# Kernel optimization log

Hardware: AMD Instinct MI355X
Metric: run time of the kernel (lower is better)

Reference implementation:

```python
import jax, jax.numpy as jnp
import numpy as np

B, T, C = 4, 2048, 1024
H = 16
D = C // H  # head_dim = 64


def setup_inputs() -> dict:
    key = jax.random.key(0)
    ks = jax.random.split(key, 11)
    s = 0.02
    return {
        "q": jax.random.normal(ks[0], (B, T, C), jnp.float32),
        "k": jax.random.normal(ks[1], (B, T, C), jnp.float32),
        "v": jax.random.normal(ks[2], (B, T, C), jnp.float32),
        "Wq": jax.random.normal(ks[3], (C, C), jnp.float32) * s,
        "bq": jnp.zeros((C,), jnp.float32),
        "Wk": jax.random.normal(ks[4], (C, C), jnp.float32) * s,
        "bk": jnp.zeros((C,), jnp.float32),
        "Wv": jax.random.normal(ks[5], (C, C), jnp.float32) * s,
        "bv": jnp.zeros((C,), jnp.float32),
        "Wo": jax.random.normal(ks[6], (C, C), jnp.float32) * s,
        "bo": jnp.zeros((C,), jnp.float32),
    }


def reference(q, k, v, Wq, bq, Wk, bk, Wv, bv, Wo, bo):
    # projections (torch Linear: x @ W.T + b)
    qh = (q @ Wq.T + bq).reshape(B, T, H, D).transpose(0, 2, 1, 3)  # [B,H,T,D]
    kh = (k @ Wk.T + bk).reshape(B, T, H, D).transpose(0, 2, 1, 3)
    vh = (v @ Wv.T + bv).reshape(B, T, H, D).transpose(0, 2, 1, 3)
    scores = jnp.einsum('bhqd,bhkd->bhqk', qh, kh) * (D ** -0.5)  # [B,H,T,T]
    # causal mask (is_causal=True)
    causal = jnp.tril(jnp.ones((T, T), bool))
    scores = jnp.where(causal, scores, -jnp.inf)
    probs = jax.nn.softmax(scores, axis=-1)
    # dropout_rate=0.0 -> identity in eval mode
    out = jnp.einsum('bhqk,bhkd->bhqd', probs, vh)  # [B,H,T,D]
    out = out.transpose(0, 2, 1, 3).reshape(B, T, C)
    return out @ Wo.T + bo
```

## Files before the change

### kernel.cpp

```cpp
#include <hip/hip_runtime.h>
#include <hip/hip_bf16.h>

typedef __attribute__((ext_vector_type(8))) short bf16x8;
typedef __attribute__((ext_vector_type(4))) float f32x4;
typedef __attribute__((ext_vector_type(16))) float f32x16;

__device__ __forceinline__ unsigned short f2bf(float x) {
  union { float f; unsigned u; } v; v.f = x;
  unsigned r = v.u + 0x7fffu + ((v.u >> 16) & 1u);
  return (unsigned short)(r >> 16);
}

__device__ __forceinline__ unsigned cvtpk_bf16(float lo, float hi) {
  unsigned r;
  asm("v_cvt_pk_bf16_f32 %0, %1, %2" : "=v"(r) : "v"(lo), "v"(hi));
  return r;
}
__device__ __forceinline__ void pl32swap(unsigned &a, unsigned &b) {
  asm volatile("v_permlane32_swap_b32 %0, %1" : "+v"(a), "+v"(b));
}
__device__ __forceinline__ void gload_lds16(const void* g, void* l) {
  __builtin_amdgcn_global_load_lds((const __attribute__((address_space(1))) void*)g,
                                   (__attribute__((address_space(3))) void*)l, 16, 0, 0);
}

#define SWZ(x) ((x) ^ ((((x) >> 7) & 7) << 4))

__global__ __launch_bounds__(256) void cvt_w(
    const float* __restrict__ W0, const float* __restrict__ W1,
    const float* __restrict__ W2, const float* __restrict__ W3,
    unsigned short* __restrict__ o0, unsigned short* __restrict__ o1,
    unsigned short* __restrict__ o2, unsigned short* __restrict__ o3,
    float s0) {
  const int z = blockIdx.y;
  const float* W = (z == 0) ? W0 : (z == 1) ? W1 : (z == 2) ? W2 : W3;
  unsigned short* o = (z == 0) ? o0 : (z == 1) ? o1 : (z == 2) ? o2 : o3;
  const float s = (z == 0) ? s0 : 1.0f;
  const int i = blockIdx.x * 256 + threadIdx.x;
  const float4 x = ((const float4*)W)[i];
  uint2 u;
  u.x = cvtpk_bf16(x.x * s, x.y * s);
  u.y = cvtpk_bf16(x.z * s, x.w * s);
  ((uint2*)o)[i] = u;
}

__global__ __launch_bounds__(256) void cvt_x(
    const float* __restrict__ q, const float* __restrict__ k,
    const float* __restrict__ v,
    unsigned short* __restrict__ oq, unsigned short* __restrict__ ok,
    unsigned short* __restrict__ ov) {
  const int z = blockIdx.y;
  const float* X = (z == 0) ? q : (z == 1) ? k : v;
  unsigned short* o = (z == 0) ? oq : (z == 1) ? ok : ov;
  const int i = blockIdx.x * 256 + threadIdx.x;
  const float4 x = ((const float4*)X)[i];
  uint2 u;
  u.x = cvtpk_bf16(x.x, x.y);
  u.y = cvtpk_bf16(x.z, x.w);
  ((uint2*)o)[i] = u;
}

__global__ __launch_bounds__(256) void proj_gemm3(
    const unsigned short* __restrict__ X0, const unsigned short* __restrict__ X1,
    const unsigned short* __restrict__ X2,
    const unsigned short* __restrict__ W0b, const unsigned short* __restrict__ W1b,
    const unsigned short* __restrict__ W2b,
    const float* __restrict__ b0, const float* __restrict__ b1, const float* __restrict__ b2,
    unsigned short* __restrict__ o0, unsigned short* __restrict__ o1,
    unsigned short* __restrict__ o2) {
  const int K = 1024;
  const int NK = 16;
  __shared__ __align__(16) unsigned short As[2][8192];
  __shared__ __align__(16) unsigned short Bs[2][8192];
  const int z = blockIdx.z;
  const unsigned short* A = (z == 0) ? X0 : (z == 1) ? X1 : X2;
  const unsigned short* Wb = (z == 0) ? W0b : (z == 1) ? W1b : W2b;
  const float* bias = (z == 0) ? b0 : (z == 1) ? b1 : b2;
  unsigned short* out = (z == 0) ? o0 : (z == 1) ? o1 : o2;
  const float bscale = (z == 0) ? 0.125f * 1.4426950408889634f : 1.0f;
  const int vtrans = (z == 2);

  const int tid = threadIdx.x;
  const int row0 = blockIdx.x * 128;
  const int col0 = blockIdx.y * 128;
  const int lane = tid & 63;
  const int w = tid >> 6;
  const int wm = (w >> 1) * 64, wn = (w & 1) * 64;
  const int fr = lane & 15;
  const int g = lane >> 4;
  const int frh = fr >> 1;
  const int gcf = ((fr & 1) * 4 + g) ^ frh;
  const int aoff = wm * 64 + frh * 128 + gcf * 16;
  const int boff = wn * 64 + frh * 128 + gcf * 16;

  const unsigned short* asrc[2];
  const unsigned short* bsrc[2];
  int ldo[2];
#pragma unroll
  for (int j = 0; j < 2; ++j) {
    const int L = (w * 2 + j) * 64 + lane;
    const int pp = L >> 3, gc = L & 7;
    const int e = gc ^ (pp & 7);
    const int r = pp * 2 + (e >> 2), c = e & 3;
    asrc[j] = A + (size_t)(row0 + r) * K + c * 8;
    bsrc[j] = Wb + (size_t)(col0 + r) * K + c * 8;
    ldo[j] = (w * 2 + j) * 1024;
  }

  f32x4 acc[4][4] = {};

  auto stage = [&](int buf, int kt) {
#pragma unroll
    for (int h = 0; h < 2; ++h)
#pragma unroll
      for (int j = 0; j < 2; ++j) {
        gload_lds16(asrc[j] + kt * 64 + h * 32, (char*)As[buf] + h * 8192 + ldo[j]);
        gload_lds16(bsrc[j] + kt * 64 + h * 32, (char*)Bs[buf] + h * 8192 + ldo[j]);
      }
  };

  stage(0, 0);
  __syncthreads();
  for (int kt = 0; kt < NK; ++kt) {
    const int buf = kt & 1;
    if (kt + 1 < NK) stage(buf ^ 1, kt + 1);
#pragma unroll
    for (int h = 0; h < 2; ++h) {
      const char* Ab = (const char*)As[buf] + h * 8192;
      const char* Bb = (const char*)Bs[buf] + h * 8192;
      bf16x8 af[4], bfv[4];
#pragma unroll
      for (int i = 0; i < 4; ++i) {
        af[i] = *(const bf16x8*)(Ab + aoff + i * 1024);
        bfv[i] = *(const bf16x8*)(Bb + boff + i * 1024);
      }
      __builtin_amdgcn_s_setprio(1);
#pragma unroll
      for (int i = 0; i < 4; ++i)
#pragma unroll
        for (int j = 0; j < 4; ++j)
          acc[i][j] = __builtin_amdgcn_mfma_f32_16x16x32_bf16(af[i], bfv[j], acc[i][j], 0, 0, 0);
      __builtin_amdgcn_s_setprio(0);
    }
    __syncthreads();
  }

#pragma unroll
  for (int j = 0; j < 4; ++j) {
    const int n = col0 + wn + j * 16 + fr;
    const float bv = bias[n] * bscale;
    const int h = n >> 6, d = n & 63;
#pragma unroll
    for (int i = 0; i < 4; ++i) {
      const int mrow = row0 + wm + i * 16 + g * 4;
      const int b = mrow >> 11, t0 = mrow & 2047;
      if (vtrans) {
        uint2 u;
        u.x = cvtpk_bf16(acc[i][j][0] + bv, acc[i][j][1] + bv);
        u.y = cvtpk_bf16(acc[i][j][2] + bv, acc[i][j][3] + bv);
        *(uint2*)(&out[(((size_t)b * 16 + h) * 64 + d) * 2048 + t0]) = u;
      } else {
#pragma unroll
        for (int r = 0; r < 4; ++r)
          out[(((size_t)b * 16 + h) * 2048 + (t0 + r)) * 64 + d] = f2bf(acc[i][j][r] + bv);
      }
    }
  }
}

__global__ __launch_bounds__(256) void out_gemm(
    const unsigned short* __restrict__ A, const unsigned short* __restrict__ Wb,
    const float* __restrict__ bias, float* __restrict__ out) {
  const int K = 1024;
  const int NK = 16;
  __shared__ __align__(16) unsigned short As[2][8192];
  __shared__ __align__(16) unsigned short Bs[2][8192];
  const int tid = threadIdx.x;
  const int row0 = blockIdx.x * 128;
  const int col0 = blockIdx.y * 128;
  const int lane = tid & 63;
  const int w = tid >> 6;
  const int wm = (w >> 1) * 64, wn = (w & 1) * 64;
  const int fr = lane & 15;
  const int g = lane >> 4;
  const int frh = fr >> 1;
  const int gcf = ((fr & 1) * 4 + g) ^ frh;
  const int aoff = wm * 64 + frh * 128 + gcf * 16;
  const int boff = wn * 64 + frh * 128 + gcf * 16;

  const unsigned short* asrc[2];
  const unsigned short* bsrc[2];
  int ldo[2];
#pragma unroll
  for (int j = 0; j < 2; ++j) {
    const int L = (w * 2 + j) * 64 + lane;
    const int pp = L >> 3, gc = L & 7;
    const int e = gc ^ (pp & 7);
    const int r = pp * 2 + (e >> 2), c = e & 3;
    asrc[j] = A + (size_t)(row0 + r) * K + c * 8;
    bsrc[j] = Wb + (size_t)(col0 + r) * K + c * 8;
    ldo[j] = (w * 2 + j) * 1024;
  }

  f32x4 acc[4][4] = {};

  auto stage = [&](int buf, int kt) {
#pragma unroll
    for (int h = 0; h < 2; ++h)
#pragma unroll
      for (int j = 0; j < 2; ++j) {
        gload_lds16(asrc[j] + kt * 64 + h * 32, (char*)As[buf] + h * 8192 + ldo[j]);
        gload_lds16(bsrc[j] + kt * 64 + h * 32, (char*)Bs[buf] + h * 8192 + ldo[j]);
      }
  };

  stage(0, 0);
  __syncthreads();
  for (int kt = 0; kt < NK; ++kt) {
    const int buf = kt & 1;
    if (kt + 1 < NK) stage(buf ^ 1, kt + 1);
#pragma unroll
    for (int h = 0; h < 2; ++h) {
      const char* Ab = (const char*)As[buf] + h * 8192;
      const char* Bb = (const char*)Bs[buf] + h * 8192;
      bf16x8 af[4], bfv[4];
#pragma unroll
      for (int i = 0; i < 4; ++i) {
        af[i] = *(const bf16x8*)(Ab + aoff + i * 1024);
        bfv[i] = *(const bf16x8*)(Bb + boff + i * 1024);
      }
      __builtin_amdgcn_s_setprio(1);
#pragma unroll
      for (int i = 0; i < 4; ++i)
#pragma unroll
        for (int j = 0; j < 4; ++j)
          acc[i][j] = __builtin_amdgcn_mfma_f32_16x16x32_bf16(af[i], bfv[j], acc[i][j], 0, 0, 0);
      __builtin_amdgcn_s_setprio(0);
    }
    __syncthreads();
  }

#pragma unroll
  for (int j = 0; j < 4; ++j) {
    const int n = col0 + wn + j * 16 + fr;
    const float bv = bias[n];
#pragma unroll
    for (int i = 0; i < 4; ++i) {
      const int mrow = row0 + wm + i * 16 + g * 4;
#pragma unroll
      for (int r = 0; r < 4; ++r)
        out[(size_t)(mrow + r) * 1024 + n] = acc[i][j][r] + bv;
    }
  }
}

__global__ __launch_bounds__(256) void attn_mfma(
    const unsigned short* __restrict__ qh, const unsigned short* __restrict__ kh,
    const unsigned short* __restrict__ vT, unsigned short* __restrict__ Ob) {
  __shared__ __align__(16) unsigned short Klds[2][64 * 64];
  __shared__ __align__(16) unsigned short Vlds[2][64 * 64];

  const int tid = threadIdx.x;
  const int lane = tid & 63;
  const int w = tid >> 6;
  const int bh = blockIdx.y;
  const int b = bh >> 4, h = bh & 15;
  const int q32 = lane & 31;
  const int hi = lane >> 5;

  const char* kbase = (const char*)(kh + (size_t)bh * 2048 * 64);
  const char* vbase = (const char*)(vT + (size_t)bh * 64 * 2048);

  const int lrow = lane >> 3;
  const int cb = (((lane & 7) ^ lrow) << 4);

  auto stage = [&](int buf, int t) {
    const int kv0 = t * 64;
#pragma unroll
    for (int j = 0; j < 2; ++j) {
      const int c = w * 2 + j;
      const int r = c * 8 + lrow;
      gload_lds16(kbase + (size_t)(kv0 + r) * 128 + cb,
                  (char*)Klds[buf] + c * 1024);
      gload_lds16(vbase + (size_t)r * 4096 + (size_t)kv0 * 2 + cb,
                  (char*)Vlds[buf] + c * 1024);
    }
  };

  const int x = (int)blockIdx.x;
  const int qt = (x < 8) ? (15 - x) : (x - 8);
  const int qb = qt * 128 + w * 32;
  const int nt = 2 * qt + 2;

  bf16x8 qf[4];
  {
    const unsigned short* qp = qh + ((size_t)bh * 2048 + qb + q32) * 64;
#pragma unroll
    for (int kk = 0; kk < 4; ++kk)
      qf[kk] = *(const bf16x8*)(qp + kk * 16 + hi * 8);
  }

  f32x16 acc_o[2] = {};
  float l_run = 0.f;

  stage(0, 0);
  __syncthreads();

  int cur = 0;
  for (int t = 0; t < nt; ++t) {
    const int kv0 = t * 64;
    if (t + 1 < nt) stage(cur ^ 1, t + 1);

    if (kv0 < qb + 32) {
      const char* Kb = (const char*)Klds[cur];
      const char* Vb = (const char*)Vlds[cur];

      f32x16 sacc[2] = {};
      __builtin_amdgcn_s_setprio(1);
#pragma unroll
      for (int kk = 0; kk < 4; ++kk) {
        bf16x8 kf0 = *(const bf16x8*)(Kb + SWZ((q32) * 128 + kk * 32 + hi * 16));
        bf16x8 kf1 = *(const bf16x8*)(Kb + SWZ((32 + q32) * 128 + kk * 32 + hi * 16));
        sacc[0] = __builtin_amdgcn_mfma_f32_32x32x16_bf16(kf0, qf[kk], sacc[0], 0, 0, 0);
        sacc[1] = __builtin_amdgcn_mfma_f32_32x32x16_bf16(kf1, qf[kk], sacc[1], 0, 0, 0);
      }
      __builtin_amdgcn_s_setprio(0);

      if (kv0 + 64 > qb) {
        const int qa = qb + q32;
#pragma unroll
        for (int mkv = 0; mkv < 2; ++mkv)
#pragma unroll
          for (int r = 0; r < 16; ++r) {
            const int kva = kv0 + mkv * 32 + 4 * hi + (r & 3) + 8 * (r >> 2);
            if (kva > qa) sacc[mkv][r] = -INFINITY;
          }
      }

      float ls = 0.f;
      unsigned W[2][8];
#pragma unroll
      for (int mkv = 0; mkv < 2; ++mkv)
#pragma unroll
        for (int s = 0; s < 8; ++s) {
          const float p0 = exp2f(sacc[mkv][2 * s]);
          const float p1 = exp2f(sacc[mkv][2 * s + 1]);
          ls += p0 + p1;
          W[mkv][s] = cvtpk_bf16(p0, p1);
        }
      ls += __shfl_xor(ls, 32);
      l_run += ls;

#pragma unroll
      for (int mkv = 0; mkv < 2; ++mkv) {
        pl32swap(W[mkv][0], W[mkv][2]);
        pl32swap(W[mkv][1], W[mkv][3]);
        pl32swap(W[mkv][4], W[mkv][6]);
        pl32swap(W[mkv][5], W[mkv][7]);
      }

      __builtin_amdgcn_s_setprio(1);
#pragma unroll
      for (int wg = 0; wg < 4; ++wg) {
        union { unsigned u[4]; bf16x8 v; } pk;
        pk.u[0] = W[wg >> 1][(wg & 1) * 4 + 0];
        pk.u[1] = W[wg >> 1][(wg & 1) * 4 + 1];
        pk.u[2] = W[wg >> 1][(wg & 1) * 4 + 2];
        pk.u[3] = W[wg >> 1][(wg & 1) * 4 + 3];
        bf16x8 vf0 = *(const bf16x8*)(Vb + SWZ((q32) * 128 + wg * 32 + hi * 16));
        bf16x8 vf1 = *(const bf16x8*)(Vb + SWZ((32 + q32) * 128 + wg * 32 + hi * 16));
        acc_o[0] = __builtin_amdgcn_mfma_f32_32x32x16_bf16(vf0, pk.v, acc_o[0], 0, 0, 0);
        acc_o[1] = __builtin_amdgcn_mfma_f32_32x32x16_bf16(vf1, pk.v, acc_o[1], 0, 0, 0);
      }
      __builtin_amdgcn_s_setprio(0);
    }

    __syncthreads();
    cur ^= 1;
  }

  {
    const float inv = 1.0f / l_run;
    const int qa = qb + q32;
    unsigned short* op = Ob + ((size_t)b * 2048 + qa) * 1024 + h * 64;
#pragma unroll
    for (int md = 0; md < 2; ++md)
#pragma unroll
      for (int rr = 0; rr < 4; ++rr) {
        uint2 u;
        u.x = cvtpk_bf16(acc_o[md][rr * 4 + 0] * inv, acc_o[md][rr * 4 + 1] * inv);
        u.y = cvtpk_bf16(acc_o[md][rr * 4 + 2] * inv, acc_o[md][rr * 4 + 3] * inv);
        *(uint2*)(op + md * 32 + rr * 8 + hi * 4) = u;
      }
  }
}

extern "C" void kernel_launch(void* const* d_in, const int* in_sizes, int n_in,
                              void* d_out, int out_size, void* d_ws, size_t ws_size,
                              hipStream_t stream) {
  (void)in_sizes; (void)n_in; (void)out_size; (void)ws_size;
  const float* q = (const float*)d_in[0];
  const float* k = (const float*)d_in[1];
  const float* v = (const float*)d_in[2];
  const float* Wq = (const float*)d_in[3];
  const float* bq = (const float*)d_in[4];
  const float* Wk = (const float*)d_in[5];
  const float* bk = (const float*)d_in[6];
  const float* Wv = (const float*)d_in[7];
  const float* bv = (const float*)d_in[8];
  const float* Wo = (const float*)d_in[9];
  const float* bo = (const float*)d_in[10];
  float* out = (float*)d_out;

  const size_t SZ = (size_t)4 * 16 * 2048 * 64;
  const size_t WSZ = (size_t)1024 * 1024;
  unsigned short* qx = (unsigned short*)d_ws;
  unsigned short* kx = qx + SZ;
  unsigned short* vx = kx + SZ;
  unsigned short* qh = vx + SZ;
  unsigned short* kh = qh + SZ;
  unsigned short* vT = kh + SZ;
  unsigned short* Wqb = vT + SZ;
  unsigned short* Wkb = Wqb + WSZ;
  unsigned short* Wvb = Wkb + WSZ;
  unsigned short* Wob = Wvb + WSZ;
  unsigned short* Ob = qx;

  dim3 g0(1024, 4), b0(256);
  cvt_w<<<g0, b0, 0, stream>>>(Wq, Wk, Wv, Wo, Wqb, Wkb, Wvb, Wob,
                               0.125f * 1.4426950408889634f);
  dim3 gx(8192, 3), bx(256);
  cvt_x<<<gx, bx, 0, stream>>>(q, k, v, qx, kx, vx);

  dim3 g1(64, 8, 3), b1(256);
  proj_gemm3<<<g1, b1, 0, stream>>>(qx, kx, vx, Wqb, Wkb, Wvb, bq, bk, bv,
                                    qh, kh, vT);

  dim3 g2(16, 64), b2(256);
  attn_mfma<<<g2, b2, 0, stream>>>(qh, kh, vT, Ob);

  dim3 g3(64, 8), b3(256);
  out_gemm<<<g3, b3, 0, stream>>>(Ob, Wob, bo, out);
}
```

Before: 248.3 us.

## Split causal attention KV range across two blocks and combine partials

Each attention block now covers a pair of query tiles (one long, one short) but only half of each tile's KV range, so the two halves run in separate blocks. Unnormalized partial outputs are stored in bf16 along with the row sums, and a new combine kernel adds the halves and normalizes. The intent is better load balance across blocks for the causal workload. In exchange it adds an extra kernel launch, the global traffic for the partials, and a second bf16 rounding of the unnormalized accumulators.

```diff
diff --git a/kernel.cpp b/kernel.cpp
--- a/kernel.cpp
+++ b/kernel.cpp
@@ -10,6 +10,8 @@
   unsigned r = v.u + 0x7fffu + ((v.u >> 16) & 1u);
   return (unsigned short)(r >> 16);
 }
+__device__ __forceinline__ float bflo(unsigned u) { union { unsigned v; float f; } x; x.v = u << 16; return x.f; }
+__device__ __forceinline__ float bfhi(unsigned u) { union { unsigned v; float f; } x; x.v = u & 0xffff0000u; return x.f; }
 
 __device__ __forceinline__ unsigned cvtpk_bf16(float lo, float hi) {
   unsigned r;
@@ -254,9 +256,11 @@
   }
 }
 
-__global__ __launch_bounds__(256) void attn_mfma(
+__global__ __launch_bounds__(256) void attn_part(
     const unsigned short* __restrict__ qh, const unsigned short* __restrict__ kh,
-    const unsigned short* __restrict__ vT, unsigned short* __restrict__ Ob) {
+    const unsigned short* __restrict__ vT,
+    unsigned short* __restrict__ Op0, unsigned short* __restrict__ Op1,
+    float* __restrict__ lp) {
   __shared__ __align__(16) unsigned short Klds[2][64 * 64];
   __shared__ __align__(16) unsigned short Vlds[2][64 * 64];
 
@@ -264,7 +268,6 @@
   const int lane = tid & 63;
   const int w = tid >> 6;
   const int bh = blockIdx.y;
-  const int b = bh >> 4, h = bh & 15;
   const int q32 = lane & 31;
   const int hi = lane >> 5;
 
@@ -288,111 +291,149 @@
   };
 
   const int x = (int)blockIdx.x;
-  const int qt = (x < 8) ? (15 - x) : (x - 8);
-  const int qb = qt * 128 + w * 32;
-  const int nt = 2 * qt + 2;
-
-  bf16x8 qf[4];
-  {
-    const unsigned short* qp = qh + ((size_t)bh * 2048 + qb + q32) * 64;
-#pragma unroll
-    for (int kk = 0; kk < 4; ++kk)
-      qf[kk] = *(const bf16x8*)(qp + kk * 16 + hi * 8);
-  }
-
-  f32x16 acc_o[2] = {};
-  float l_run = 0.f;
-
-  stage(0, 0);
-  __syncthreads();
-
-  int cur = 0;
-  for (int t = 0; t < nt; ++t) {
-    const int kv0 = t * 64;
-    if (t + 1 < nt) stage(cur ^ 1, t + 1);
-
-    if (kv0 < qb + 32) {
-      const char* Kb = (const char*)Klds[cur];
-      const char* Vb = (const char*)Vlds[cur];
-
-      f32x16 sacc[2] = {};
-      __builtin_amdgcn_s_setprio(1);
-#pragma unroll
-      for (int kk = 0; kk < 4; ++kk) {
-        bf16x8 kf0 = *(const bf16x8*)(Kb + SWZ((q32) * 128 + kk * 32 + hi * 16));
-        bf16x8 kf1 = *(const bf16x8*)(Kb + SWZ((32 + q32) * 128 + kk * 32 + hi * 16));
-        sacc[0] = __builtin_amdgcn_mfma_f32_32x32x16_bf16(kf0, qf[kk], sacc[0], 0, 0, 0);
-        sacc[1] = __builtin_amdgcn_mfma_f32_32x32x16_bf16(kf1, qf[kk], sacc[1], 0, 0, 0);
-      }
-      __builtin_amdgcn_s_setprio(0);
-
-      if (kv0 + 64 > qb) {
-        const int qa = qb + q32;
+  const int x8 = x & 7;
+  const int half = x >> 3;
+  unsigned short* Op = half ? Op1 : Op0;
+  float* lph = lp + (size_t)half * (64 * 2048);
+
+  for (int seg = 0; seg < 2; ++seg) {
+    const int qt = (seg == 0) ? (15 - x8) : x8;
+    const int qb = qt * 128 + w * 32;
+    const int t0 = (half == 0) ? 0 : (qt + 1);
+    const int t1 = (half == 0) ? (qt + 1) : (2 * qt + 2);
+
+    bf16x8 qf[4];
+    {
+      const unsigned short* qp = qh + ((size_t)bh * 2048 + qb + q32) * 64;
+#pragma unroll
+      for (int kk = 0; kk < 4; ++kk)
+        qf[kk] = *(const bf16x8*)(qp + kk * 16 + hi * 8);
+    }
+
+    f32x16 acc_o[2] = {};
+    float l_run = 0.f;
+
+    stage(0, t0);
+    __syncthreads();
+
+    int cur = 0;
+    for (int t = t0; t < t1; ++t) {
+      const int kv0 = t * 64;
+      if (t + 1 < t1) stage(cur ^ 1, t + 1);
+
+      if (kv0 < qb + 32) {
+        const char* Kb = (const char*)Klds[cur];
+        const char* Vb = (const char*)Vlds[cur];
+
+        f32x16 sacc[2] = {};
+        __builtin_amdgcn_s_setprio(1);
+#pragma unroll
+        for (int kk = 0; kk < 4; ++kk) {
+          bf16x8 kf0 = *(const bf16x8*)(Kb + SWZ((q32) * 128 + kk * 32 + hi * 16));
+          bf16x8 kf1 = *(const bf16x8*)(Kb + SWZ((32 + q32) * 128 + kk * 32 + hi * 16));
+          sacc[0] = __builtin_amdgcn_mfma_f32_32x32x16_bf16(kf0, qf[kk], sacc[0], 0, 0, 0);
+          sacc[1] = __builtin_amdgcn_mfma_f32_32x32x16_bf16(kf1, qf[kk], sacc[1], 0, 0, 0);
+        }
+        __builtin_amdgcn_s_setprio(0);
+
+        if (kv0 + 64 > qb) {
+          const int qa = qb + q32;
+#pragma unroll
+          for (int mkv = 0; mkv < 2; ++mkv)
+#pragma unroll
+            for (int r = 0; r < 16; ++r) {
+              const int kva = kv0 + mkv * 32 + 4 * hi + (r & 3) + 8 * (r >> 2);
+              if (kva > qa) sacc[mkv][r] = -INFINITY;
+            }
+        }
+
+        float ls = 0.f;
+        unsigned W[2][8];
 #pragma unroll
         for (int mkv = 0; mkv < 2; ++mkv)
 #pragma unroll
-          for (int r = 0; r < 16; ++r) {
-            const int kva = kv0 + mkv * 32 + 4 * hi + (r & 3) + 8 * (r >> 2);
-            if (kva > qa) sacc[mkv][r] = -INFINITY;
+          for (int s = 0; s < 8; ++s) {
+            const float p0 = exp2f(sacc[mkv][2 * s]);
+            const float p1 = exp2f(sacc[mkv][2 * s + 1]);
+            ls += p0 + p1;
+            W[mkv][s] = cvtpk_bf16(p0, p1);
           }
-      }
-
-      float ls = 0.f;
-      unsigned W[2][8];
-#pragma unroll
-      for (int mkv = 0; mkv < 2; ++mkv)
-#pragma unroll
-        for (int s = 0; s < 8; ++s) {
-          const float p0 = exp2f(sacc[mkv][2 * s]);
-          const float p1 = exp2f(sacc[mkv][2 * s + 1]);
-          ls += p0 + p1;
-          W[mkv][s] = cvtpk_bf16(p0, p1);
+        ls += __shfl_xor(ls, 32);
+        l_run += ls;
+
+#pragma unroll
+        for (int mkv = 0; mkv < 2; ++mkv) {
+          pl32swap(W[mkv][0], W[mkv][2]);
+          pl32swap(W[mkv][1], W[mkv][3]);
+          pl32swap(W[mkv][4], W[mkv][6]);
+          pl32swap(W[mkv][5], W[mkv][7]);
         }
-      ls += __shfl_xor(ls, 32);
-      l_run += ls;
-
-#pragma unroll
-      for (int mkv = 0; mkv < 2; ++mkv) {
-        pl32swap(W[mkv][0], W[mkv][2]);
-        pl32swap(W[mkv][1], W[mkv][3]);
-        pl32swap(W[mkv][4], W[mkv][6]);
-        pl32swap(W[mkv][5], W[mkv][7]);
-      }
-
-      __builtin_amdgcn_s_setprio(1);
-#pragma unroll
-      for (int wg = 0; wg < 4; ++wg) {
-        union { unsigned u[4]; bf16x8 v; } pk;
-        pk.u[0] = W[wg >> 1][(wg & 1) * 4 + 0];
-        pk.u[1] = W[wg >> 1][(wg & 1) * 4 + 1];
-        pk.u[2] = W[wg >> 1][(wg & 1) * 4 + 2];
-        pk.u[3] = W[wg >> 1][(wg & 1) * 4 + 3];
-        bf16x8 vf0 = *(const bf16x8*)(Vb + SWZ((q32) * 128 + wg * 32 + hi * 16));
-        bf16x8 vf1 = *(const bf16x8*)(Vb + SWZ((32 + q32) * 128 + wg * 32 + hi * 16));
-        acc_o[0] = __builtin_amdgcn_mfma_f32_32x32x16_bf16(vf0, pk.v, acc_o[0], 0, 0, 0);
-        acc_o[1] = __builtin_amdgcn_mfma_f32_32x32x16_bf16(vf1, pk.v, acc_o[1], 0, 0, 0);
-      }
-      __builtin_amdgcn_s_setprio(0);
-    }
-
-    __syncthreads();
-    cur ^= 1;
-  }
-
-  {
-    const float inv = 1.0f / l_run;
-    const int qa = qb + q32;
-    unsigned short* op = Ob + ((size_t)b * 2048 + qa) * 1024 + h * 64;
-#pragma unroll
-    for (int md = 0; md < 2; ++md)
-#pragma unroll
-      for (int rr = 0; rr < 4; ++rr) {
-        uint2 u;
-        u.x = cvtpk_bf16(acc_o[md][rr * 4 + 0] * inv, acc_o[md][rr * 4 + 1] * inv);
-        u.y = cvtpk_bf16(acc_o[md][rr * 4 + 2] * inv, acc_o[md][rr * 4 + 3] * inv);
-        *(uint2*)(op + md * 32 + rr * 8 + hi * 4) = u;
-      }
-  }
+
+        __builtin_amdgcn_s_setprio(1);
+#pragma unroll
+        for (int wg = 0; wg < 4; ++wg) {
+          union { unsigned u[4]; bf16x8 v; } pk;
+          pk.u[0] = W[wg >> 1][(wg & 1) * 4 + 0];
+          pk.u[1] = W[wg >> 1][(wg & 1) * 4 + 1];
+          pk.u[2] = W[wg >> 1][(wg & 1) * 4 + 2];
+          pk.u[3] = W[wg >> 1][(wg & 1) * 4 + 3];
+          bf16x8 vf0 = *(const bf16x8*)(Vb + SWZ((q32) * 128 + wg * 32 + hi * 16));
+          bf16x8 vf1 = *(const bf16x8*)(Vb + SWZ((32 + q32) * 128 + wg * 32 + hi * 16));
+          acc_o[0] = __builtin_amdgcn_mfma_f32_32x32x16_bf16(vf0, pk.v, acc_o[0], 0, 0, 0);
+          acc_o[1] = __builtin_amdgcn_mfma_f32_32x32x16_bf16(vf1, pk.v, acc_o[1], 0, 0, 0);
+        }
+        __builtin_amdgcn_s_setprio(0);
+      }
+
+      __syncthreads();
+      cur ^= 1;
+    }
+
+    {
+      const int qa = qb + q32;
+      unsigned short* op = Op + ((size_t)bh * 2048 + qa) * 64;
+#pragma unroll
+      for (int md = 0; md < 2; ++md)
+#pragma unroll
+        for (int rr = 0; rr < 4; ++rr) {
+          uint2 u;
+          u.x = cvtpk_bf16(acc_o[md][rr * 4 + 0], acc_o[md][rr * 4 + 1]);
+          u.y = cvtpk_bf16(acc_o[md][rr * 4 + 2], acc_o[md][rr * 4 + 3]);
+          *(uint2*)(op + md * 32 + rr * 8 + hi * 4) = u;
+        }
+      if (hi == 0) lph[bh * 2048 + qa] = l_run;
+    }
+  }
+}
+
+__global__ __launch_bounds__(256) void attn_combine(
+    const unsigned short* __restrict__ Op0, const unsigned short* __restrict__ Op1,
+    const float* __restrict__ lp, unsigned short* __restrict__ Ob) {
+  const int gi = blockIdx.x * 256 + threadIdx.x;
+  const int c = gi & 3;
+  const int q = (gi >> 2) & 2047;
+  const int bh = gi >> 13;
+  const int b = bh >> 4, h = bh & 15;
+  const float l0 = lp[bh * 2048 + q];
+  const float l1 = lp[64 * 2048 + bh * 2048 + q];
+  const float inv = 1.0f / (l0 + l1);
+  const size_t off = ((size_t)bh * 2048 + q) * 64 + c * 16;
+  const uint4 a0 = *(const uint4*)(Op0 + off);
+  const uint4 a1 = *(const uint4*)(Op0 + off + 8);
+  const uint4 c0 = *(const uint4*)(Op1 + off);
+  const uint4 c1 = *(const uint4*)(Op1 + off + 8);
+  unsigned short* op = Ob + ((size_t)b * 2048 + q) * 1024 + h * 64 + c * 16;
+  uint4 r0, r1;
+  r0.x = cvtpk_bf16((bflo(a0.x) + bflo(c0.x)) * inv, (bfhi(a0.x) + bfhi(c0.x)) * inv);
+  r0.y = cvtpk_bf16((bflo(a0.y) + bflo(c0.y)) * inv, (bfhi(a0.y) + bfhi(c0.y)) * inv);
+  r0.z = cvtpk_bf16((bflo(a0.z) + bflo(c0.z)) * inv, (bfhi(a0.z) + bfhi(c0.z)) * inv);
+  r0.w = cvtpk_bf16((bflo(a0.w) + bflo(c0.w)) * inv, (bfhi(a0.w) + bfhi(c0.w)) * inv);
+  r1.x = cvtpk_bf16((bflo(a1.x) + bflo(c1.x)) * inv, (bfhi(a1.x) + bfhi(c1.x)) * inv);
+  r1.y = cvtpk_bf16((bflo(a1.y) + bflo(c1.y)) * inv, (bfhi(a1.y) + bfhi(c1.y)) * inv);
+  r1.z = cvtpk_bf16((bflo(a1.z) + bflo(c1.z)) * inv, (bfhi(a1.z) + bfhi(c1.z)) * inv);
+  r1.w = cvtpk_bf16((bflo(a1.w) + bflo(c1.w)) * inv, (bfhi(a1.w) + bfhi(c1.w)) * inv);
+  *(uint4*)op = r0;
+  *(uint4*)(op + 8) = r1;
 }
 
 extern "C" void kernel_launch(void* const* d_in, const int* in_sizes, int n_in,
@@ -404,8 +445,8 @@
   const float* v = (const float*)d_in[2];
   const float* Wq = (const float*)d_in[3];
   const float* bq = (const float*)d_in[4];
+  const float* bk = (const float*)d_in[6];
   const float* Wk = (const float*)d_in[5];
-  const float* bk = (const float*)d_in[6];
   const float* Wv = (const float*)d_in[7];
   const float* bv = (const float*)d_in[8];
   const float* Wo = (const float*)d_in[9];
@@ -424,6 +465,9 @@
   unsigned short* Wkb = Wqb + WSZ;
   unsigned short* Wvb = Wkb + WSZ;
   unsigned short* Wob = Wvb + WSZ;
+  float* lp = (float*)(Wob + WSZ);
+  unsigned short* Op0 = kx;
+  unsigned short* Op1 = vx;
   unsigned short* Ob = qx;
 
   dim3 g0(1024, 4), b0(256);
@@ -437,7 +481,9 @@
                                     qh, kh, vT);
 
   dim3 g2(16, 64), b2(256);
-  attn_mfma<<<g2, b2, 0, stream>>>(qh, kh, vT, Ob);
+  attn_part<<<g2, b2, 0, stream>>>(qh, kh, vT, Op0, Op1, lp);
+  dim3 g2c(2048), b2c(256);
+  attn_combine<<<g2c, b2c, 0, stream>>>(Op0, Op1, lp, Ob);
 
   dim3 g3(64, 8), b3(256);
   out_gemm<<<g3, b3, 0, stream>>>(Ob, Wob, bo, out);
```

Result: faster. 218.5 us (-12.0%).
